# Kernel tuning notes

Measured on AMD Instinct MI355X. Metric: run time of the kernel, lower is better.

## Reference

```python
import jax, jax.numpy as jnp
import numpy as np

N_NODES = 50000


def gcn_conv(x, src, dst, W, b, n_nodes):
    # PyG GCNConv: add self-loops, symmetric normalization D^-1/2 (A+I) D^-1/2 (x W) + b
    E = src.shape[0]
    deg = jax.ops.segment_sum(jnp.ones((E,), x.dtype), dst, num_segments=n_nodes) + 1.0
    dinv = jax.lax.rsqrt(deg)
    h = x @ W  # [N, H]
    norm = dinv[src] * dinv[dst]  # [E]
    agg = jax.ops.segment_sum(h[src] * norm[:, None], dst, num_segments=n_nodes)
    agg = agg + h * (dinv * dinv)[:, None]  # self-loop contribution
    return agg + b


def setup_inputs() -> dict:
    key = jax.random.key(0)
    ks = jax.random.split(key, 16)
    N, E, D, H, T, O = N_NODES, 800000, 128, 128, 2, 1
    x = jax.random.normal(ks[0], (N, D), jnp.float32)
    edge_index = jax.random.randint(ks[1], (2, E), 0, N, jnp.int32)
    edge_attrs = jax.random.uniform(ks[2], (T, E, 7), jnp.float32)
    s = lambda k, sh: jax.random.normal(k, sh, jnp.float32) * (1.0 / np.sqrt(sh[0]))
    return {
        "x": x, "edge_index": edge_index, "edge_attrs": edge_attrs,
        "W1": s(ks[3], (D, H)), "b1": jnp.zeros((H,), jnp.float32),
        "W2": s(ks[4], (H, H)), "b2": jnp.zeros((H,), jnp.float32),
        "W3": s(ks[5], (H, H)), "b3": jnp.zeros((H,), jnp.float32),
        "We": s(ks[6], (2 * H + 7, H)), "be": jnp.zeros((H,), jnp.float32),
        "Wg": s(ks[7], (H, O)), "bg": jnp.zeros((O,), jnp.float32),
    }


def reference(x, edge_index, edge_attrs, W1, b1, W2, b2, W3, b3, We, be, Wg, bg):
    src, dst = edge_index[0], edge_index[1]
    n = x.shape[0]
    outputs = []
    for t in range(edge_attrs.shape[0]):  # small fixed T, x evolves across iterations
        edge_attr = edge_attrs[t]
        x = jax.nn.relu(gcn_conv(x, src, dst, W1, b1, n))
        x = jax.nn.relu(gcn_conv(x, src, dst, W2, b2, n))
        x = jax.nn.relu(gcn_conv(x, src, dst, W3, b3, n))
        # gather-concat-MLP-mean per edge
        edge_features = jnp.concatenate([x[src], x[dst], edge_attr], axis=1)
        edge_output = jax.nn.relu(edge_features @ We + be)
        graph_features = jnp.mean(edge_output, axis=0, keepdims=True)  # [1, H]
        outputs.append(graph_features @ Wg + bg)
        W1 = W2  # no-op placeholder removed below
        W1 = W1  # keep W1 unchanged
    return jnp.concatenate(outputs, axis=0)  # [T, output_dim]
```

## Files before the change

### kernel.cpp

```cpp
#include <hip/hip_runtime.h>
#include <hip/hip_bf16.h>


typedef __attribute__((ext_vector_type(8))) short bf16x8;
typedef __attribute__((ext_vector_type(4))) float f32x4;
typedef __attribute__((ext_vector_type(2))) float f32x2;

__device__ __forceinline__ unsigned short f2bf(float f) {
    union { float f; unsigned int u; } v; v.f = f;
    unsigned int r = v.u + 0x7fffu + ((v.u >> 16) & 1u);
    return (unsigned short)(r >> 16);
}
__device__ __forceinline__ unsigned int pk2bf(float lo, float hi) {
    return (unsigned int)f2bf(lo) | ((unsigned int)f2bf(hi) << 16);
}
__device__ __forceinline__ unsigned char f2fp8(float f) {
    return (unsigned char)(__builtin_amdgcn_cvt_pk_fp8_f32(f, f, 0, false) & 0xff);
}
__device__ __forceinline__ f32x2 max0_2(f32x2 v) {
#if __has_builtin(__builtin_elementwise_max)
    return __builtin_elementwise_max(v, (f32x2){0.f, 0.f});
#else
    return (f32x2){fmaxf(v[0], 0.f), fmaxf(v[1], 0.f)};
#endif
}

__global__ void to_bf16(const float* __restrict__ in, unsigned short* __restrict__ out, int n4)
{
    int i = blockIdx.x * 256 + threadIdx.x;
    if (i < n4) {
        float4 v = ((const float4*)in)[i];
        ushort4 o;
        o.x = f2bf(v.x); o.y = f2bf(v.y); o.z = f2bf(v.z); o.w = f2bf(v.w);
        ((ushort4*)out)[i] = o;
    }
}

__global__ void transpose_w(
    const float* __restrict__ W1, const float* __restrict__ W2,
    const float* __restrict__ W3, const float* __restrict__ We,
    unsigned short* __restrict__ T1, unsigned short* __restrict__ T2,
    unsigned short* __restrict__ T3, unsigned short* __restrict__ Tuv)
{
    const float* src; unsigned short* dst;
    switch (blockIdx.y) {
        case 0:  src = W1;             dst = T1;               break;
        case 1:  src = W2;             dst = T2;               break;
        case 2:  src = W3;             dst = T3;               break;
        case 3:  src = We;             dst = Tuv;              break;
        case 4:  src = We + 128 * 128; dst = Tuv + 128 * 128;  break;
        default: src = W2;             dst = Tuv + 256 * 128;  break;
    }
    for (int i = blockIdx.x * 256 + threadIdx.x; i < 128 * 128; i += 256 * gridDim.x) {
        int k = i >> 7, c = i & 127;
        dst[c * 128 + k] = f2bf(src[i]);
    }
}

__global__ __launch_bounds__(256) void mfma_matmul(
    const unsigned short* __restrict__ X, const unsigned short* __restrict__ Wt,
    unsigned char* __restrict__ out, const float* __restrict__ scale, int n_rows)
{
    const int wave = threadIdx.x >> 6;
    const int lane = threadIdx.x & 63;
    const int m = lane & 15;
    const int q = lane >> 4;
    const int r = blockIdx.x * 64 + wave * 16 + m;
    const bool rv = r < n_rows;

    f32x4 acc[8];
    #pragma unroll
    for (int i = 0; i < 8; ++i) acc[i] = (f32x4){0.f, 0.f, 0.f, 0.f};

    #pragma unroll
    for (int k0 = 0; k0 < 128; k0 += 32) {
        bf16x8 a = {};
        if (rv) a = *(const bf16x8*)(X + (size_t)r * 128 + k0 + q * 8);
        #pragma unroll
        for (int ct = 0; ct < 8; ++ct) {
            bf16x8 b = *(const bf16x8*)(Wt + (ct * 16 + m) * 128 + k0 + q * 8);
            acc[ct] = __builtin_amdgcn_mfma_f32_16x16x32_bf16(a, b, acc[ct], 0, 0, 0);
        }
    }

    #pragma unroll
    for (int reg = 0; reg < 4; ++reg) {
        int gr = blockIdx.x * 64 + wave * 16 + q * 4 + reg;
        if (gr >= n_rows) continue;
        float s = scale[gr];
        #pragma unroll
        for (int ct = 0; ct < 8; ++ct)
            out[(size_t)gr * 128 + ct * 16 + m] = f2fp8(acc[ct][reg] * s);
    }
}

#define GNODES 8
#define ICAP 64
#define ISTR 72
#define GATHER_LDS (GNODES * ISTR * 4)
#define EM_CHUNK 256
#define EDGE_LDS 10240

__device__ __forceinline__ void gather_body(
    int bx, int* idxl,
    const unsigned char* __restrict__ hs_in, const int* __restrict__ csr_src,
    const int* __restrict__ offs, const int* __restrict__ counts,
    const float* __restrict__ dinv, const float* __restrict__ bias,
    unsigned short* __restrict__ xout, int n)
{
    const int tid = threadIdx.x;
    const int row = tid >> 5;
    const int node = bx * GNODES + row;
    const int lg = tid & 31;
    const int c4 = lg * 4;

    if (node >= n) return;
    const int off = offs[node];
    const int cnt = counts[node];
    const int cap = min(cnt, ICAP);

    for (int j = lg; j < cap; j += 32)
        idxl[row * ISTR + j] = csr_src[off + j];

    const unsigned int sv = *(const unsigned int*)(hs_in + (size_t)node * 128 + c4);

    f32x2 a01 = {0.f, 0.f}, a23 = {0.f, 0.f};
    auto de4 = [&](unsigned int v) {
        a01 += __builtin_amdgcn_cvt_pk_f32_fp8(v, false);
        a23 += __builtin_amdgcn_cvt_pk_f32_fp8(v, true);
    };
    unsigned int A[4], B[4];
    auto LQ = [&](unsigned int* Q, int jb) {
        #pragma unroll
        for (int q = 0; q < 4; ++q)
            Q[q] = *(const unsigned int*)(hs_in + (size_t)idxl[row * ISTR + jb + q] * 128 + c4);
    };
    auto CONS = [&](unsigned int* Q) {
        #pragma unroll
        for (int q = 0; q < 4; ++q) de4(Q[q]);
    };

    int j = 0;
    if (cap >= 8) {
        LQ(A, 0); LQ(B, 4);
        de4(sv);
        j = 8;
        for (; j + 8 <= cap; j += 8) {
            CONS(A); LQ(A, j);
            CONS(B); LQ(B, j + 4);
        }
        CONS(A); CONS(B);
    } else if (cap >= 4) {
        LQ(A, 0);
        de4(sv);
        CONS(A);
        j = 4;
    } else {
        de4(sv);
    }
    if (j + 4 <= cap) {
        LQ(A, j); CONS(A); j += 4;
    }
    for (; j < cap; ++j)
        de4(*(const unsigned int*)(hs_in + (size_t)idxl[row * ISTR + j] * 128 + c4));
    for (; j < cnt; ++j)
        de4(*(const unsigned int*)(hs_in + (size_t)csr_src[off + j] * 128 + c4));

    const float dn = dinv[node];
    const float4 bb = *(const float4*)(bias + c4);
    float r0 = fmaxf(fmaf(a01[0], dn, bb.x), 0.f);
    float r1 = fmaxf(fmaf(a01[1], dn, bb.y), 0.f);
    float r2 = fmaxf(fmaf(a23[0], dn, bb.z), 0.f);
    float r3 = fmaxf(fmaf(a23[1], dn, bb.w), 0.f);
    uint2 w;
    w.x = pk2bf(r0, r1); w.y = pk2bf(r2, r3);
    *(uint2*)(xout + (size_t)node * 128 + c4) = w;
}

__global__ __launch_bounds__(256, 8) void gather_relu(
    const unsigned char* __restrict__ hs_in, const int* __restrict__ csr_src,
    const int* __restrict__ offs, const int* __restrict__ counts,
    const float* __restrict__ dinv, const float* __restrict__ bias,
    unsigned short* __restrict__ xout, int n)
{
    __shared__ int idxl[GNODES * ISTR];
    gather_body(blockIdx.x, idxl, hs_in, csr_src, offs, counts, dinv, bias, xout, n);
}

__global__ __launch_bounds__(256) void matmul_cols(
    const unsigned short* __restrict__ X, const unsigned short* __restrict__ Wt,
    int uvcols, unsigned char* __restrict__ buv, unsigned char* __restrict__ bh,
    const float* __restrict__ dinv, int n_rows)
{
    const int wave = threadIdx.x >> 6;
    const int lane = threadIdx.x & 63;
    const int m = lane & 15;
    const int q = lane >> 4;
    const int r = blockIdx.x * 64 + wave * 16 + m;
    const bool rv = r < n_rows;
    const int cg = blockIdx.y;
    const unsigned short* Wc = Wt + (size_t)cg * 128 * 128;

    f32x4 acc[8];
    #pragma unroll
    for (int i = 0; i < 8; ++i) acc[i] = (f32x4){0.f, 0.f, 0.f, 0.f};

    #pragma unroll
    for (int k0 = 0; k0 < 128; k0 += 32) {
        bf16x8 a = {};
        if (rv) a = *(const bf16x8*)(X + (size_t)r * 128 + k0 + q * 8);
        #pragma unroll
        for (int ct = 0; ct < 8; ++ct) {
            bf16x8 b = *(const bf16x8*)(Wc + (ct * 16 + m) * 128 + k0 + q * 8);
            acc[ct] = __builtin_amdgcn_mfma_f32_16x16x32_bf16(a, b, acc[ct], 0, 0, 0);
        }
    }

    #pragma unroll
    for (int reg = 0; reg < 4; ++reg) {
        int gr = blockIdx.x * 64 + wave * 16 + q * 4 + reg;
        if (gr >= n_rows) continue;
        #pragma unroll
        for (int ct = 0; ct < 8; ++ct) {
            int col = cg * 128 + ct * 16 + m;
            if (col < uvcols)
                buv[(size_t)gr * 256 + col] = f2fp8(acc[ct][reg]);
            else
                bh[(size_t)gr * 128 + col - uvcols] = f2fp8(acc[ct][reg] * dinv[gr]);
        }
    }
}

__device__ __forceinline__ void edge_body(
    int bx, int nbx, char* smem,
    const unsigned char* __restrict__ uv, const int* __restrict__ src,
    const int* __restrict__ dst, const float* __restrict__ ea,
    const float* __restrict__ We_e, const float* __restrict__ be,
    const float* __restrict__ Wg, float* __restrict__ acc, int E)
{
    float* eas = (float*)smem;
    int*   ss  = (int*)(smem + 7168);
    int*   ds  = (int*)(smem + 8192);
    float* red = (float*)(smem + 9216);

    const int tid  = threadIdx.x;
    const int lane = tid & 31;
    const int g    = tid >> 5;
    const int c4   = lane * 4;

    f32x2 wlo[7], whi[7];
    #pragma unroll
    for (int i = 0; i < 7; ++i) {
        float4 wv = *(const float4*)(We_e + i * 128 + c4);
        wlo[i] = (f32x2){wv.x, wv.y};
        whi[i] = (f32x2){wv.z, wv.w};
    }
    const float4 bev = *(const float4*)(be + c4);
    const f32x2 be01 = (f32x2){bev.x, bev.y};
    const f32x2 be23 = (f32x2){bev.z, bev.w};
    const float4 wg4 = *(const float4*)(Wg + c4);

    f32x2 part01 = {0.f, 0.f}, part23 = {0.f, 0.f};

    for (int base = bx * EM_CHUNK; base < E; base += nbx * EM_CHUNK) {
        const int nch = min(EM_CHUNK, E - base);
        for (int i = tid; i < nch * 7; i += 256)
            eas[i] = ea[(size_t)base * 7 + i];
        for (int i = tid; i < nch; i += 256) {
            ss[i] = src[base + i];
            ds[i] = dst[base + i];
        }
        __syncthreads();

        auto ev = [&](int j) {
            unsigned int us = *(const unsigned int*)(uv + (size_t)ss[j] * 256 + c4);
            unsigned int vs = *(const unsigned int*)(uv + (size_t)ds[j] * 256 + 128 + c4);
            f32x2 u01 = __builtin_amdgcn_cvt_pk_f32_fp8(us, false);
            f32x2 u23 = __builtin_amdgcn_cvt_pk_f32_fp8(us, true);
            f32x2 v01 = __builtin_amdgcn_cvt_pk_f32_fp8(vs, false);
            f32x2 v23 = __builtin_amdgcn_cvt_pk_f32_fp8(vs, true);
            f32x2 val01 = u01 + v01 + be01;
            f32x2 val23 = u23 + v23 + be23;
            const float* eav = &eas[j * 7];
            #pragma unroll
            for (int i = 0; i < 7; ++i) {
                f32x2 e2 = (f32x2){eav[i], eav[i]};
                val01 += e2 * wlo[i];
                val23 += e2 * whi[i];
            }
            part01 += max0_2(val01);
            part23 += max0_2(val23);
        };

        int j = g;
        for (; j + 32 <= nch; j += 32) {
            ev(j); ev(j + 8); ev(j + 16); ev(j + 24);
        }
        for (; j < nch; j += 8)
            ev(j);
        __syncthreads();
    }

    float p = part01[0] * wg4.x + part01[1] * wg4.y + part23[0] * wg4.z + part23[1] * wg4.w;
    red[tid] = p;
    __syncthreads();
    for (int s = 128; s > 0; s >>= 1) {
        if (tid < s) red[tid] += red[tid + s];
        __syncthreads();
    }
    if (tid == 0) atomicAdd(acc, red[0]);
}

__global__ __launch_bounds__(256) void edge_mlp(
    const unsigned char* __restrict__ uv, const int* __restrict__ src,
    const int* __restrict__ dst, const float* __restrict__ ea,
    const float* __restrict__ We_e, const float* __restrict__ be,
    const float* __restrict__ Wg, float* __restrict__ acc, int E)
{
    __shared__ __align__(16) char smem[EDGE_LDS];
    edge_body(blockIdx.x, gridDim.x, smem, uv, src, dst, ea, We_e, be, Wg, acc, E);
}

__global__ __launch_bounds__(256, 8) void gather_edge(
    int ng,
    const unsigned char* __restrict__ hs_in, const int* __restrict__ csr_src,
    const int* __restrict__ offs, const int* __restrict__ counts,
    const float* __restrict__ dinv, const float* __restrict__ bias,
    unsigned short* __restrict__ xout, int n,
    int ne,
    const unsigned char* __restrict__ uv, const int* __restrict__ src,
    const int* __restrict__ dst, const float* __restrict__ ea,
    const float* __restrict__ We_e, const float* __restrict__ be,
    const float* __restrict__ Wg, float* __restrict__ acc, int E)
{
    __shared__ __align__(16) char smem[EDGE_LDS];
    const int bid = blockIdx.x;
    const int full = min(ng >> 4, ne >> 3);
    const int inter = full * 24;
    int role, idx;
    if (bid < inter) {
        int gp = bid / 24, r = bid % 24;
        if (r < 16) { role = 0; idx = gp * 16 + r; }
        else        { role = 1; idx = gp * 8 + (r - 16); }
    } else {
        int rr = bid - inter;
        int gleft = ng - full * 16;
        if (rr < gleft) { role = 0; idx = full * 16 + rr; }
        else            { role = 1; idx = full * 8 + (rr - gleft); }
    }
    if (role == 0)
        gather_body(idx, (int*)smem, hs_in, csr_src, offs, counts, dinv, bias, xout, n);
    else
        edge_body(idx, ne, smem, uv, src, dst, ea, We_e, be, Wg, acc, E);
}

__global__ void count_edges(const int* __restrict__ dst, int* __restrict__ counts,
                            int* __restrict__ rank, int E)
{
    int e = blockIdx.x * 256 + threadIdx.x;
    if (e < E) rank[e] = atomicAdd(&counts[dst[e]], 1);
}

__global__ void scan1(const int* __restrict__ counts, int* __restrict__ scanned,
                      int* __restrict__ btot, float* __restrict__ dinv, int n)
{
    __shared__ int sh[256];
    int i = blockIdx.x * 256 + threadIdx.x;
    int v = (i < n) ? counts[i] : 0;
    if (i < n) dinv[i] = rsqrtf((float)v + 1.0f);
    sh[threadIdx.x] = v;
    __syncthreads();
    for (int off = 1; off < 256; off <<= 1) {
        int t = (threadIdx.x >= off) ? sh[threadIdx.x - off] : 0;
        __syncthreads();
        sh[threadIdx.x] += t;
        __syncthreads();
    }
    if (i < n) scanned[i] = sh[threadIdx.x] - v;
    if (threadIdx.x == 255) btot[blockIdx.x] = sh[255];
}

__global__ void scan2(int* __restrict__ btot, int nb)
{
    __shared__ int sh[256];
    int v = (threadIdx.x < nb) ? btot[threadIdx.x] : 0;
    sh[threadIdx.x] = v;
    __syncthreads();
    for (int off = 1; off < 256; off <<= 1) {
        int t = (threadIdx.x >= off) ? sh[threadIdx.x - off] : 0;
        __syncthreads();
        sh[threadIdx.x] += t;
        __syncthreads();
    }
    if (threadIdx.x < nb) btot[threadIdx.x] = sh[threadIdx.x] - v;
}

__global__ void scan3(const int* __restrict__ scanned, const int* __restrict__ btot,
                      int* __restrict__ offs, int n)
{
    int i = blockIdx.x * 256 + threadIdx.x;
    if (i < n) offs[i] = scanned[i] + btot[blockIdx.x];
}

__global__ void fill_csr2(const int* __restrict__ src, const int* __restrict__ dst,
                          const int* __restrict__ rank, const int* __restrict__ offs,
                          int* __restrict__ csr_src, int E, int n)
{
    const int g8 = blockIdx.x & 7;
    const int b8 = blockIdx.x >> 3;
    const int nb8 = gridDim.x >> 3;
    const int chunk = (n + 7) >> 3;
    const int lo = g8 * chunk;
    const int hi = min(n, lo + chunk);
    for (int e = b8 * 256 + threadIdx.x; e < E; e += nb8 * 256) {
        int d = dst[e];
        if (d >= lo && d < hi)
            csr_src[offs[d] + rank[e]] = src[e];
    }
}

__global__ void write_out(const float* __restrict__ acc, const float* __restrict__ bg,
                          float* __restrict__ out, float invE, int T)
{
    int t = threadIdx.x;
    if (t < T) out[t] = acc[t] * invE + bg[0];
}


extern "C" void kernel_launch(void* const* d_in, const int* in_sizes, int n_in,
                              void* d_out, int out_size, void* d_ws, size_t ws_size,
                              hipStream_t stream)
{
    const float* x   = (const float*)d_in[0];
    const int*  eidx = (const int*)d_in[1];
    const float* ea  = (const float*)d_in[2];
    const float* W1  = (const float*)d_in[3];
    const float* b1  = (const float*)d_in[4];
    const float* W2  = (const float*)d_in[5];
    const float* b2  = (const float*)d_in[6];
    const float* W3  = (const float*)d_in[7];
    const float* b3  = (const float*)d_in[8];
    const float* We  = (const float*)d_in[9];
    const float* be  = (const float*)d_in[10];
    const float* Wg  = (const float*)d_in[11];
    const float* bg  = (const float*)d_in[12];

    const int N = in_sizes[0] / 128;
    const int E = in_sizes[1] / 2;
    const int T = in_sizes[2] / (E * 7);
    const int* src = eidx;
    const int* dst = eidx + E;

    char* wsp = (char*)d_ws;
    auto alloc = [&](size_t bytes) -> char* {
        char* p = wsp;
        wsp += (bytes + 255) / 256 * 256;
        return p;
    };
    int*   counts  = (int*)alloc((size_t)N * 4);
    int*   offs    = (int*)alloc((size_t)N * 4);
    int*   scanned = (int*)alloc((size_t)N * 4);
    int*   btot    = (int*)alloc(1024);
    int*   rank    = (int*)alloc((size_t)E * 4);
    int*   csr_src = (int*)alloc((size_t)E * 4);
    float* dinv    = (float*)alloc((size_t)N * 4);
    float* acc     = (float*)alloc(256);
    unsigned short* X0  = (unsigned short*)alloc((size_t)N * 128 * 2);
    unsigned char*  Bh0 = (unsigned char*)alloc((size_t)N * 128);
    unsigned char*  Bh1 = (unsigned char*)alloc((size_t)N * 128);
    unsigned char*  Buv = (unsigned char*)alloc((size_t)N * 256);
    unsigned short* T1  = (unsigned short*)alloc(128 * 128 * 2);
    unsigned short* T2  = (unsigned short*)alloc(128 * 128 * 2);
    unsigned short* T3  = (unsigned short*)alloc(128 * 128 * 2);
    unsigned short* Tuv = (unsigned short*)alloc(384 * 128 * 2);

    hipMemsetAsync(counts, 0, (size_t)N * 4, stream);
    hipMemsetAsync(acc, 0, (size_t)T * 4, stream);

    to_bf16<<<(N * 128 / 4 + 255) / 256, 256, 0, stream>>>(x, X0, N * 128 / 4);
    transpose_w<<<dim3(8, 6), 256, 0, stream>>>(W1, W2, W3, We, T1, T2, T3, Tuv);

    count_edges<<<(E + 255) / 256, 256, 0, stream>>>(dst, counts, rank, E);
    const int nb = (N + 255) / 256;
    scan1<<<nb, 256, 0, stream>>>(counts, scanned, btot, dinv, N);
    scan2<<<1, 256, 0, stream>>>(btot, nb);
    scan3<<<nb, 256, 0, stream>>>(scanned, btot, offs, N);
    fill_csr2<<<2048, 256, 0, stream>>>(src, dst, rank, offs, csr_src, E, N);

    const int mmb = (N + 63) / 64;
    const int ngb = (N + GNODES - 1) / GNODES;
    const int emb = (E + EM_CHUNK - 1) / EM_CHUNK;

    unsigned char* hcur = Bh0;
    unsigned char* hnxt = Bh1;
    auto swap = [&]() { unsigned char* tmp = hcur; hcur = hnxt; hnxt = tmp; };

    mfma_matmul<<<mmb, 256, 0, stream>>>(X0, T1, hcur, dinv, N);
    gather_relu<<<ngb, 256, 0, stream>>>(hcur, csr_src, offs, counts, dinv, b1, X0, N);
    matmul_cols<<<dim3(mmb, 1), 256, 0, stream>>>(X0, T2, 0, Buv, hnxt, dinv, N);
    swap();
    gather_relu<<<ngb, 256, 0, stream>>>(hcur, csr_src, offs, counts, dinv, b2, X0, N);
    matmul_cols<<<dim3(mmb, 1), 256, 0, stream>>>(X0, T3, 0, Buv, hnxt, dinv, N);
    swap();

    for (int t = 0; t < T; ++t) {
        const bool last = (t == T - 1);
        gather_relu<<<ngb, 256, 0, stream>>>(hcur, csr_src, offs, counts, dinv, b3, X0, N);
        matmul_cols<<<dim3(mmb, last ? 2 : 3), 256, 0, stream>>>(
            X0, Tuv, 256, Buv, hnxt, dinv, N);
        if (last) {
            edge_mlp<<<emb, 256, 0, stream>>>(Buv, src, dst, ea + (size_t)t * E * 7,
                                              We + 256 * 128, be, Wg, acc + t, E);
        } else {
            swap();
            gather_edge<<<ngb + emb, 256, 0, stream>>>(
                ngb, hcur, csr_src, offs, counts, dinv, b1, X0, N,
                emb, Buv, src, dst, ea + (size_t)t * E * 7,
                We + 256 * 128, be, Wg, acc + t, E);
            matmul_cols<<<dim3(mmb, 1), 256, 0, stream>>>(X0, T2, 0, Buv, hnxt, dinv, N);
            swap();
            gather_relu<<<ngb, 256, 0, stream>>>(hcur, csr_src, offs, counts, dinv, b2, X0, N);
            matmul_cols<<<dim3(mmb, 1), 256, 0, stream>>>(X0, T3, 0, Buv, hnxt, dinv, N);
            swap();
        }
    }
    write_out<<<1, 64, 0, stream>>>(acc, bg, (float*)d_out, 1.0f / (float)E, T);
}
```

Before: 609.8 us.

## Split neighbor gather into two channel-half passes and drop fused gather/edge kernel

The neighbor aggregation is split into two launches that each handle 64 of the 128 feature channels, using 16 nodes per block with 16 lanes per node. This halves the footprint of the fp8 feature table touched per pass, likely to improve cache hit rates on the random gathers. CSR index loads and bf16 output stores become nontemporal. The combined gather+edge-MLP kernel that overlapped layer-1 gather with the edge MLP is removed, so the edge MLP now runs as its own launch and the CSR index lists are read twice per layer.

```diff
diff --git a/kernel.cpp b/kernel.cpp
--- a/kernel.cpp
+++ b/kernel.cpp
@@ -94,33 +94,32 @@
     }
 }
 
-#define GNODES 8
+#define GH_NODES 16
 #define ICAP 64
 #define ISTR 72
-#define GATHER_LDS (GNODES * ISTR * 4)
 #define EM_CHUNK 256
 #define EDGE_LDS 10240
 
-__device__ __forceinline__ void gather_body(
-    int bx, int* idxl,
+__global__ __launch_bounds__(256, 8) void gather_half(
     const unsigned char* __restrict__ hs_in, const int* __restrict__ csr_src,
     const int* __restrict__ offs, const int* __restrict__ counts,
     const float* __restrict__ dinv, const float* __restrict__ bias,
-    unsigned short* __restrict__ xout, int n)
-{
+    unsigned short* __restrict__ xout, int ch0, int n)
+{
+    __shared__ int idxl[GH_NODES * ISTR];
     const int tid = threadIdx.x;
-    const int row = tid >> 5;
-    const int node = bx * GNODES + row;
-    const int lg = tid & 31;
-    const int c4 = lg * 4;
+    const int row = tid >> 4;
+    const int node = blockIdx.x * GH_NODES + row;
+    const int lg = tid & 15;
+    const int c4 = ch0 + lg * 4;
 
     if (node >= n) return;
     const int off = offs[node];
     const int cnt = counts[node];
     const int cap = min(cnt, ICAP);
 
-    for (int j = lg; j < cap; j += 32)
-        idxl[row * ISTR + j] = csr_src[off + j];
+    for (int j = lg; j < cap; j += 16)
+        idxl[row * ISTR + j] = __builtin_nontemporal_load(csr_src + off + j);
 
     const unsigned int sv = *(const unsigned int*)(hs_in + (size_t)node * 128 + c4);
 
@@ -172,19 +171,9 @@
     float r1 = fmaxf(fmaf(a01[1], dn, bb.y), 0.f);
     float r2 = fmaxf(fmaf(a23[0], dn, bb.z), 0.f);
     float r3 = fmaxf(fmaf(a23[1], dn, bb.w), 0.f);
-    uint2 w;
-    w.x = pk2bf(r0, r1); w.y = pk2bf(r2, r3);
-    *(uint2*)(xout + (size_t)node * 128 + c4) = w;
-}
-
-__global__ __launch_bounds__(256, 8) void gather_relu(
-    const unsigned char* __restrict__ hs_in, const int* __restrict__ csr_src,
-    const int* __restrict__ offs, const int* __restrict__ counts,
-    const float* __restrict__ dinv, const float* __restrict__ bias,
-    unsigned short* __restrict__ xout, int n)
-{
-    __shared__ int idxl[GNODES * ISTR];
-    gather_body(blockIdx.x, idxl, hs_in, csr_src, offs, counts, dinv, bias, xout, n);
+    unsigned long long w = (unsigned long long)pk2bf(r0, r1)
+                         | ((unsigned long long)pk2bf(r2, r3) << 32);
+    __builtin_nontemporal_store(w, (unsigned long long*)(xout + (size_t)node * 128 + c4));
 }
 
 __global__ __launch_bounds__(256) void matmul_cols(
@@ -231,13 +220,13 @@
     }
 }
 
-__device__ __forceinline__ void edge_body(
-    int bx, int nbx, char* smem,
+__global__ __launch_bounds__(256) void edge_mlp(
     const unsigned char* __restrict__ uv, const int* __restrict__ src,
     const int* __restrict__ dst, const float* __restrict__ ea,
     const float* __restrict__ We_e, const float* __restrict__ be,
     const float* __restrict__ Wg, float* __restrict__ acc, int E)
 {
+    __shared__ __align__(16) char smem[EDGE_LDS];
     float* eas = (float*)smem;
     int*   ss  = (int*)(smem + 7168);
     int*   ds  = (int*)(smem + 8192);
@@ -262,7 +251,7 @@
 
     f32x2 part01 = {0.f, 0.f}, part23 = {0.f, 0.f};
 
-    for (int base = bx * EM_CHUNK; base < E; base += nbx * EM_CHUNK) {
+    for (int base = blockIdx.x * EM_CHUNK; base < E; base += gridDim.x * EM_CHUNK) {
         const int nch = min(EM_CHUNK, E - base);
         for (int i = tid; i < nch * 7; i += 256)
             eas[i] = ea[(size_t)base * 7 + i];
@@ -309,49 +298,6 @@
         __syncthreads();
     }
     if (tid == 0) atomicAdd(acc, red[0]);
-}
-
-__global__ __launch_bounds__(256) void edge_mlp(
-    const unsigned char* __restrict__ uv, const int* __restrict__ src,
-    const int* __restrict__ dst, const float* __restrict__ ea,
-    const float* __restrict__ We_e, const float* __restrict__ be,
-    const float* __restrict__ Wg, float* __restrict__ acc, int E)
-{
-    __shared__ __align__(16) char smem[EDGE_LDS];
-    edge_body(blockIdx.x, gridDim.x, smem, uv, src, dst, ea, We_e, be, Wg, acc, E);
-}
-
-__global__ __launch_bounds__(256, 8) void gather_edge(
-    int ng,
-    const unsigned char* __restrict__ hs_in, const int* __restrict__ csr_src,
-    const int* __restrict__ offs, const int* __restrict__ counts,
-    const float* __restrict__ dinv, const float* __restrict__ bias,
-    unsigned short* __restrict__ xout, int n,
-    int ne,
-    const unsigned char* __restrict__ uv, const int* __restrict__ src,
-    const int* __restrict__ dst, const float* __restrict__ ea,
-    const float* __restrict__ We_e, const float* __restrict__ be,
-    const float* __restrict__ Wg, float* __restrict__ acc, int E)
-{
-    __shared__ __align__(16) char smem[EDGE_LDS];
-    const int bid = blockIdx.x;
-    const int full = min(ng >> 4, ne >> 3);
-    const int inter = full * 24;
-    int role, idx;
-    if (bid < inter) {
-        int gp = bid / 24, r = bid % 24;
-        if (r < 16) { role = 0; idx = gp * 16 + r; }
-        else        { role = 1; idx = gp * 8 + (r - 16); }
-    } else {
-        int rr = bid - inter;
-        int gleft = ng - full * 16;
-        if (rr < gleft) { role = 0; idx = full * 16 + rr; }
-        else            { role = 1; idx = full * 8 + (rr - gleft); }
-    }
-    if (role == 0)
-        gather_body(idx, (int*)smem, hs_in, csr_src, offs, counts, dinv, bias, xout, n);
-    else
-        edge_body(idx, ne, smem, uv, src, dst, ea, We_e, be, Wg, acc, E);
 }
 
 __global__ void count_edges(const int* __restrict__ dst, int* __restrict__ counts,
@@ -488,7 +434,7 @@
     fill_csr2<<<2048, 256, 0, stream>>>(src, dst, rank, offs, csr_src, E, N);
 
     const int mmb = (N + 63) / 64;
-    const int ngb = (N + GNODES - 1) / GNODES;
+    const int ghb = (N + GH_NODES - 1) / GH_NODES;
     const int emb = (E + EM_CHUNK - 1) / EM_CHUNK;
 
     unsigned char* hcur = Bh0;
@@ -496,33 +442,24 @@
     auto swap = [&]() { unsigned char* tmp = hcur; hcur = hnxt; hnxt = tmp; };
 
     mfma_matmul<<<mmb, 256, 0, stream>>>(X0, T1, hcur, dinv, N);
-    gather_relu<<<ngb, 256, 0, stream>>>(hcur, csr_src, offs, counts, dinv, b1, X0, N);
-    matmul_cols<<<dim3(mmb, 1), 256, 0, stream>>>(X0, T2, 0, Buv, hnxt, dinv, N);
-    swap();
-    gather_relu<<<ngb, 256, 0, stream>>>(hcur, csr_src, offs, counts, dinv, b2, X0, N);
-    matmul_cols<<<dim3(mmb, 1), 256, 0, stream>>>(X0, T3, 0, Buv, hnxt, dinv, N);
-    swap();
 
     for (int t = 0; t < T; ++t) {
         const bool last = (t == T - 1);
-        gather_relu<<<ngb, 256, 0, stream>>>(hcur, csr_src, offs, counts, dinv, b3, X0, N);
+        gather_half<<<ghb, 256, 0, stream>>>(hcur, csr_src, offs, counts, dinv, b1, X0, 0, N);
+        gather_half<<<ghb, 256, 0, stream>>>(hcur, csr_src, offs, counts, dinv, b1, X0, 64, N);
+        matmul_cols<<<dim3(mmb, 1), 256, 0, stream>>>(X0, T2, 0, Buv, hnxt, dinv, N);
+        swap();
+        gather_half<<<ghb, 256, 0, stream>>>(hcur, csr_src, offs, counts, dinv, b2, X0, 0, N);
+        gather_half<<<ghb, 256, 0, stream>>>(hcur, csr_src, offs, counts, dinv, b2, X0, 64, N);
+        matmul_cols<<<dim3(mmb, 1), 256, 0, stream>>>(X0, T3, 0, Buv, hnxt, dinv, N);
+        swap();
+        gather_half<<<ghb, 256, 0, stream>>>(hcur, csr_src, offs, counts, dinv, b3, X0, 0, N);
+        gather_half<<<ghb, 256, 0, stream>>>(hcur, csr_src, offs, counts, dinv, b3, X0, 64, N);
         matmul_cols<<<dim3(mmb, last ? 2 : 3), 256, 0, stream>>>(
             X0, Tuv, 256, Buv, hnxt, dinv, N);
-        if (last) {
-            edge_mlp<<<emb, 256, 0, stream>>>(Buv, src, dst, ea + (size_t)t * E * 7,
-                                              We + 256 * 128, be, Wg, acc + t, E);
-        } else {
-            swap();
-            gather_edge<<<ngb + emb, 256, 0, stream>>>(
-                ngb, hcur, csr_src, offs, counts, dinv, b1, X0, N,
-                emb, Buv, src, dst, ea + (size_t)t * E * 7,
-                We + 256 * 128, be, Wg, acc + t, E);
-            matmul_cols<<<dim3(mmb, 1), 256, 0, stream>>>(X0, T2, 0, Buv, hnxt, dinv, N);
-            swap();
-            gather_relu<<<ngb, 256, 0, stream>>>(hcur, csr_src, offs, counts, dinv, b2, X0, N);
-            matmul_cols<<<dim3(mmb, 1), 256, 0, stream>>>(X0, T3, 0, Buv, hnxt, dinv, N);
-            swap();
-        }
+        edge_mlp<<<emb, 256, 0, stream>>>(Buv, src, dst, ea + (size_t)t * E * 7,
+                                          We + 256 * 128, be, Wg, acc + t, E);
+        if (!last) swap();
     }
     write_out<<<1, 64, 0, stream>>>(acc, bg, (float*)d_out, 1.0f / (float)E, T);
 }
```

Measured after the change: 669.0 us. 1.1x slower.
